# Kernel optimization log

Measured on AMD Instinct MI355X. Metric: run time of the kernel, lower is better.

Reference implementation:

```python
import jax, jax.numpy as jnp
import numpy as np

E = 8        # n_experts
TOP_K = 2    # top_k_experts


def setup_inputs() -> dict:
    key = jax.random.key(0)
    ks = jax.random.split(key, 4)
    B, N, D, H = 4, 2048, 1024, 1024
    s_d = 1.0 / np.sqrt(D)
    s_h = 1.0 / np.sqrt(H)
    return {
        "x": jax.random.normal(ks[0], (B, N, D), dtype=jnp.float32),
        "router_w": jax.random.normal(ks[1], (E, D), dtype=jnp.float32) * s_d,
        "router_b": jnp.zeros((E,), dtype=jnp.float32),
        "W_up": jax.random.normal(ks[2], (E, D, H), dtype=jnp.float32) * s_d,
        "b_up": jnp.zeros((E, H), dtype=jnp.float32),
        "W_down": jax.random.normal(ks[3], (E, H, D), dtype=jnp.float32) * s_h,
        "b_down": jnp.zeros((E, D), dtype=jnp.float32),
    }


def reference(x, router_w, router_b, W_up, b_up, W_down, b_down):
    # Router logits: (B, N, E)
    logits = jnp.einsum("bnd,ed->bne", x, router_w) + router_b
    _, topk_idx = jax.lax.top_k(logits, TOP_K)          # (B, N, K)
    # Boolean mask of selected experts: (B, N, E)
    mask = jax.nn.one_hot(topk_idx, E, dtype=jnp.bool_).any(axis=-2)
    masked_logits = jnp.where(mask, logits, -jnp.inf)
    router_weights = jax.nn.softmax(masked_logits, axis=-1)  # zeros off top-k
    # Dense all-experts FFN: (B, N, E, H) intermediate
    h = jnp.einsum("bnd,edh->bneh", x, W_up) + b_up
    h = jax.nn.gelu(h, approximate=False)  # torch F.gelu default = exact erf
    h = jnp.einsum("bneh,ehd->bned", h, W_down) + b_down
    output = jnp.einsum("bne,bned->bnd", router_weights, h)
    # Switch load-balancing aux loss (dropout is identity in eval)
    f_i = mask.astype(x.dtype).mean(axis=(0, 1))
    P_i = router_weights.mean(axis=(0, 1))
    aux_loss = E * jnp.sum(f_i * P_i)
    return output, aux_loss
```

## Files before the change

kernel.cpp:

```cpp
#include <hip/hip_runtime.h>
#include <hip/hip_bf16.h>

typedef __attribute__((ext_vector_type(8))) short bf16x8_t;
typedef __attribute__((ext_vector_type(4))) float f32x4_t;

__device__ __forceinline__ void gld16(void* lds, const void* g) {
    __builtin_amdgcn_global_load_lds(
        (const __attribute__((address_space(1))) void*)g,
        (__attribute__((address_space(3))) void*)lds, 16, 0, 0);
}

__device__ inline unsigned short f2bf(float f) {
    __hip_bfloat16 h = __float2bfloat16(f);
    return *reinterpret_cast<unsigned short*>(&h);
}

__global__ __launch_bounds__(256) void transpose_kernel(
    const float* __restrict__ Wup, const float* __restrict__ Wdn,
    ushort* __restrict__ WtUp, ushort* __restrict__ WtDn)
{
    int z = blockIdx.z;
    const float* src = (z < 8) ? (Wup + ((size_t)z << 20)) : (Wdn + ((size_t)(z - 8) << 20));
    ushort* dst      = (z < 8) ? (WtUp + ((size_t)z << 20)) : (WtDn + ((size_t)(z - 8) << 20));
    __shared__ float tile[64][65];
    int x0 = blockIdx.x * 64, y0 = blockIdx.y * 64;
    int row = threadIdx.x >> 4, colq = threadIdx.x & 15;
#pragma unroll
    for (int it = 0; it < 4; it++) {
        int r = row + it * 16;
        float4 v = *(const float4*)(src + (size_t)(y0 + r) * 1024 + x0 + colq * 4);
        tile[r][colq * 4 + 0] = v.x; tile[r][colq * 4 + 1] = v.y;
        tile[r][colq * 4 + 2] = v.z; tile[r][colq * 4 + 3] = v.w;
    }
    __syncthreads();
#pragma unroll
    for (int it = 0; it < 4; it++) {
        int r = row + it * 16;
        ushort4 o;
        o.x = f2bf(tile[colq * 4 + 0][r]); o.y = f2bf(tile[colq * 4 + 1][r]);
        o.z = f2bf(tile[colq * 4 + 2][r]); o.w = f2bf(tile[colq * 4 + 3][r]);
        *(ushort4*)(dst + (size_t)(x0 + r) * 1024 + y0 + colq * 4) = o;
    }
}

__global__ __launch_bounds__(256) void router_kernel(
    const float* __restrict__ x, const float* __restrict__ rw,
    const float* __restrict__ rb, ushort* __restrict__ xb,
    int2* __restrict__ tok_e, float2* __restrict__ tok_w)
{
    int wave = threadIdx.x >> 6, lane = threadIdx.x & 63;
    int t = blockIdx.x * 4 + wave;
    float4 xv[4];
#pragma unroll
    for (int i = 0; i < 4; i++)
        xv[i] = *(const float4*)(x + (size_t)t * 1024 + i * 256 + lane * 4);
#pragma unroll
    for (int i = 0; i < 4; i++) {
        ushort4 o;
        o.x = f2bf(xv[i].x); o.y = f2bf(xv[i].y); o.z = f2bf(xv[i].z); o.w = f2bf(xv[i].w);
        *(ushort4*)(xb + (size_t)t * 1024 + i * 256 + lane * 4) = o;
    }
    float logit[8];
#pragma unroll
    for (int e = 0; e < 8; e++) {
        float s = 0.f;
#pragma unroll
        for (int i = 0; i < 4; i++) {
            float4 wv = *(const float4*)(rw + e * 1024 + i * 256 + lane * 4);
            s += xv[i].x * wv.x + xv[i].y * wv.y + xv[i].z * wv.z + xv[i].w * wv.w;
        }
#pragma unroll
        for (int m = 32; m >= 1; m >>= 1) s += __shfl_xor(s, m, 64);
        logit[e] = s + rb[e];
    }
    int i0 = 0;
#pragma unroll
    for (int e = 1; e < 8; e++) if (logit[e] > logit[i0]) i0 = e;
    int i1 = -1;
#pragma unroll
    for (int e = 0; e < 8; e++) if (e != i0 && (i1 < 0 || logit[e] > logit[i1])) i1 = e;
    float ev = expf(logit[i1] - logit[i0]);
    float s = 1.f + ev;
    if (lane == 0) {
        tok_e[t] = make_int2(i0, i1);
        tok_w[t] = make_float2(1.f / s, ev / s);
    }
}

__global__ __launch_bounds__(256) void count_kernel(
    const int2* __restrict__ tok_e, const float2* __restrict__ tok_w,
    int* __restrict__ blockCnt, float* __restrict__ blockSum)
{
    __shared__ int lcnt[8];
    __shared__ float lsum[8];
    int tid = threadIdx.x;
    if (tid < 8) { lcnt[tid] = 0; lsum[tid] = 0.f; }
    __syncthreads();
    int t = blockIdx.x * 256 + tid;
    int2 e = tok_e[t]; float2 w = tok_w[t];
    atomicAdd(&lcnt[e.x], 1); atomicAdd(&lsum[e.x], w.x);
    atomicAdd(&lcnt[e.y], 1); atomicAdd(&lsum[e.y], w.y);
    __syncthreads();
    if (tid < 8) {
        blockCnt[blockIdx.x * 8 + tid] = lcnt[tid];
        blockSum[blockIdx.x * 8 + tid] = lsum[tid];
    }
}

__global__ void scan_kernel(const int* __restrict__ blockCnt,
                            const float* __restrict__ blockSum,
                            int* __restrict__ cnt, int* __restrict__ off,
                            int* __restrict__ base, int* __restrict__ tileE,
                            int* __restrict__ tileRow, int* __restrict__ nTiles,
                            float* aux_out)
{
    if (threadIdx.x == 0) {
        int tot[8]; float sw[8];
        for (int e = 0; e < 8; e++) { tot[e] = 0; sw[e] = 0.f; }
        for (int b = 0; b < 32; b++)
            for (int e = 0; e < 8; e++) { tot[e] += blockCnt[b * 8 + e]; sw[e] += blockSum[b * 8 + e]; }
        int o = 0; float aux = 0.f; int nT = 0;
        for (int e = 0; e < 8; e++) {
            cnt[e] = tot[e]; off[e] = o;
            aux += (float)tot[e] * sw[e];
            int run = o;
            for (int b = 0; b < 32; b++) { base[b * 8 + e] = run; run += blockCnt[b * 8 + e]; }
            for (int tt = 0; tt * 128 < tot[e]; tt++) { tileE[nT] = e; tileRow[nT] = o + tt * 128; nT++; }
            o += tot[e];
        }
        *nTiles = nT;
        aux *= 8.0f / (8192.0f * 8192.0f);
        *aux_out = aux;
    }
}

__global__ __launch_bounds__(256) void assign_kernel(
    const int2* __restrict__ tok_e, const float2* __restrict__ tok_w,
    const int* __restrict__ base, int* __restrict__ pair_token,
    float* __restrict__ pair_w, int2* __restrict__ tokSlot)
{
    __shared__ int lcnt[8];
    int tid = threadIdx.x;
    if (tid < 8) lcnt[tid] = 0;
    __syncthreads();
    int t = blockIdx.x * 256 + tid;
    int2 e = tok_e[t]; float2 w = tok_w[t];
    int r0 = atomicAdd(&lcnt[e.x], 1);
    int r1 = atomicAdd(&lcnt[e.y], 1);
    int s0 = base[blockIdx.x * 8 + e.x] + r0;
    int s1 = base[blockIdx.x * 8 + e.y] + r1;
    pair_token[s0] = t; pair_w[s0] = w.x;
    pair_token[s1] = t; pair_w[s1] = w.y;
    tokSlot[t] = make_int2(s0, s1);
}

__global__ __launch_bounds__(512, 4) void up_gemm(
    const ushort* __restrict__ xb, const ushort* __restrict__ WtUp,
    const float* __restrict__ bup,
    const int* __restrict__ cnt, const int* __restrict__ off,
    const int* __restrict__ nTiles, const int* __restrict__ tileE,
    const int* __restrict__ tileRow,
    const int* __restrict__ pair_token, const float* __restrict__ pair_w,
    const ushort* __restrict__ zeroPage, ushort* __restrict__ Hbuf)
{
    if ((int)blockIdx.y >= *nTiles) return;
    int e = tileE[blockIdx.y];
    int rowBase = tileRow[blockIdx.y];
    int expertEnd = off[e] + cnt[e];
    int colBase = blockIdx.x * 128;
    const ushort* Bsrc = WtUp + ((size_t)e << 20);

    __shared__ ushort As[128 * 32];
    __shared__ ushort Bs[128 * 32];

    int tid = threadIdx.x, w = tid >> 6, lane = tid & 63;
    int q = lane >> 4, r = lane & 15;
    int wm = w & 3, wn = w >> 2;

    int sr = lane >> 2;
    int cOff = (lane & 3) * 8;
    int rA = w * 16 + sr;
    int gA = rowBase + rA;

    const ushort* aP = (gA < expertEnd) ? xb + (size_t)pair_token[gA] * 1024 + cOff : zeroPage + cOff;
    const ushort* bP = Bsrc + (size_t)(colBase + rA) * 1024 + cOff;

    ushort* lA = &As[(w * 16) * 32];
    ushort* lB = &Bs[(w * 16) * 32];

    f32x4_t acc[2][4];
#pragma unroll
    for (int i = 0; i < 2; i++)
#pragma unroll
        for (int j = 0; j < 4; j++) { acc[i][j][0] = 0.f; acc[i][j][1] = 0.f; acc[i][j][2] = 0.f; acc[i][j][3] = 0.f; }

    for (int kk = 0; kk < 1024; kk += 32) {
        gld16(lA, aP + kk);
        gld16(lB, bP + kk);
        __syncthreads();
        bf16x8_t a[2], b[4];
#pragma unroll
        for (int i = 0; i < 2; i++) a[i] = *(const bf16x8_t*)&As[(wm * 32 + i * 16 + r) * 32 + q * 8];
#pragma unroll
        for (int j = 0; j < 4; j++) b[j] = *(const bf16x8_t*)&Bs[(wn * 64 + j * 16 + r) * 32 + q * 8];
#pragma unroll
        for (int i = 0; i < 2; i++)
#pragma unroll
            for (int j = 0; j < 4; j++)
                acc[i][j] = __builtin_amdgcn_mfma_f32_16x16x32_bf16(a[i], b[j], acc[i][j], 0, 0, 0);
        __syncthreads();
    }

#pragma unroll
    for (int j = 0; j < 4; j++) {
        int col = colBase + wn * 64 + j * 16 + r;
        float bias = bup[e * 1024 + col];
#pragma unroll
        for (int i = 0; i < 2; i++) {
#pragma unroll
            for (int reg = 0; reg < 4; reg++) {
                int gRow = rowBase + wm * 32 + i * 16 + q * 4 + reg;
                if (gRow < expertEnd) {
                    float h = acc[i][j][reg] + bias;
                    float g = 0.5f * h * (1.0f + erff(h * 0.70710678118654752f));
                    Hbuf[(size_t)gRow * 1024 + col] = f2bf(g * pair_w[gRow]);
                }
            }
        }
    }
}

__global__ __launch_bounds__(512, 4) void down_gemm(
    const ushort* __restrict__ Hbuf, const ushort* __restrict__ WtDn,
    const int* __restrict__ cnt, const int* __restrict__ off,
    const int* __restrict__ nTiles, const int* __restrict__ tileE,
    const int* __restrict__ tileRow,
    const ushort* __restrict__ zeroPage, ushort* __restrict__ pairOut)
{
    if ((int)blockIdx.y >= *nTiles) return;
    int e = tileE[blockIdx.y];
    int rowBase = tileRow[blockIdx.y];
    int expertEnd = off[e] + cnt[e];
    int colBase = blockIdx.x * 128;
    const ushort* Bsrc = WtDn + ((size_t)e << 20);

    __shared__ ushort As[128 * 32];
    __shared__ ushort Bs[128 * 32];

    int tid = threadIdx.x, w = tid >> 6, lane = tid & 63;
    int q = lane >> 4, r = lane & 15;
    int wm = w & 3, wn = w >> 2;

    int sr = lane >> 2;
    int cOff = (lane & 3) * 8;
    int rA = w * 16 + sr;
    int gA = rowBase + rA;

    const ushort* aP = (gA < expertEnd) ? Hbuf + (size_t)gA * 1024 + cOff : zeroPage + cOff;
    const ushort* bP = Bsrc + (size_t)(colBase + rA) * 1024 + cOff;

    ushort* lA = &As[(w * 16) * 32];
    ushort* lB = &Bs[(w * 16) * 32];

    f32x4_t acc[2][4];
#pragma unroll
    for (int i = 0; i < 2; i++)
#pragma unroll
        for (int j = 0; j < 4; j++) { acc[i][j][0] = 0.f; acc[i][j][1] = 0.f; acc[i][j][2] = 0.f; acc[i][j][3] = 0.f; }

    for (int kk = 0; kk < 1024; kk += 32) {
        gld16(lA, aP + kk);
        gld16(lB, bP + kk);
        __syncthreads();
        bf16x8_t a[2], b[4];
#pragma unroll
        for (int i = 0; i < 2; i++) a[i] = *(const bf16x8_t*)&As[(wm * 32 + i * 16 + r) * 32 + q * 8];
#pragma unroll
        for (int j = 0; j < 4; j++) b[j] = *(const bf16x8_t*)&Bs[(wn * 64 + j * 16 + r) * 32 + q * 8];
#pragma unroll
        for (int i = 0; i < 2; i++)
#pragma unroll
            for (int j = 0; j < 4; j++)
                acc[i][j] = __builtin_amdgcn_mfma_f32_16x16x32_bf16(a[i], b[j], acc[i][j], 0, 0, 0);
        __syncthreads();
    }

#pragma unroll
    for (int j = 0; j < 4; j++) {
        int col = colBase + wn * 64 + j * 16 + r;
#pragma unroll
        for (int i = 0; i < 2; i++) {
#pragma unroll
            for (int reg = 0; reg < 4; reg++) {
                int gRow = rowBase + wm * 32 + i * 16 + q * 4 + reg;
                if (gRow < expertEnd)
                    pairOut[(size_t)gRow * 1024 + col] = f2bf(acc[i][j][reg]);
            }
        }
    }
}

__global__ __launch_bounds__(256) void finalize_kernel(
    const ushort* __restrict__ pairOut, const int2* __restrict__ tokSlot,
    const int2* __restrict__ tok_e, const float2* __restrict__ tok_w,
    const float* __restrict__ bdn, float* __restrict__ out)
{
    int t = blockIdx.x;
    int2 s = tokSlot[t]; int2 e = tok_e[t]; float2 w = tok_w[t];
    int c = threadIdx.x * 4;
    ushort4 p0 = *(const ushort4*)(pairOut + (size_t)s.x * 1024 + c);
    ushort4 p1 = *(const ushort4*)(pairOut + (size_t)s.y * 1024 + c);
    float4 b0 = *(const float4*)(bdn + (size_t)e.x * 1024 + c);
    float4 b1 = *(const float4*)(bdn + (size_t)e.y * 1024 + c);
    __hip_bfloat16* h0 = (__hip_bfloat16*)&p0;
    __hip_bfloat16* h1 = (__hip_bfloat16*)&p1;
    float4 o;
    o.x = __bfloat162float(h0[0]) + __bfloat162float(h1[0]) + w.x * b0.x + w.y * b1.x;
    o.y = __bfloat162float(h0[1]) + __bfloat162float(h1[1]) + w.x * b0.y + w.y * b1.y;
    o.z = __bfloat162float(h0[2]) + __bfloat162float(h1[2]) + w.x * b0.z + w.y * b1.z;
    o.w = __bfloat162float(h0[3]) + __bfloat162float(h1[3]) + w.x * b0.w + w.y * b1.w;
    *(float4*)(out + (size_t)t * 1024 + c) = o;
}

extern "C" void kernel_launch(void* const* d_in, const int* in_sizes, int n_in,
                              void* d_out, int out_size, void* d_ws, size_t ws_size,
                              hipStream_t stream) {
    const float* x   = (const float*)d_in[0];
    const float* rw  = (const float*)d_in[1];
    const float* rb  = (const float*)d_in[2];
    const float* Wup = (const float*)d_in[3];
    const float* bup = (const float*)d_in[4];
    const float* Wdn = (const float*)d_in[5];
    const float* bdn = (const float*)d_in[6];
    float* out = (float*)d_out;

    char* ws = (char*)d_ws;
    int*    cnt      = (int*)(ws + 0);
    int*    off      = (int*)(ws + 64);
    int*    nTiles   = (int*)(ws + 128);
    int*    blockCnt = (int*)(ws + 256);
    float*  blockSum = (float*)(ws + 1536);
    int*    base     = (int*)(ws + 2816);
    int*    tileE    = (int*)(ws + 4096);
    int*    tileRow  = (int*)(ws + 4736);
    ushort* zeroPage = (ushort*)(ws + 8192);
    int2*   tok_e    = (int2*)(ws + 12288);
    float2* tok_w    = (float2*)(ws + 77824);
    int2*   tokSlot  = (int2*)(ws + 143360);
    int*    pair_token = (int*)(ws + 208896);
    float*  pair_w     = (float*)(ws + 274432);
    char* big = ws + 1048576;
    ushort* Hbuf    = (ushort*)big;
    ushort* pairOut = (ushort*)(big + 33554432);
    ushort* WtUp    = (ushort*)(big + 67108864);
    ushort* WtDn    = (ushort*)(big + 83886080);
    ushort* xb      = (ushort*)(big + 100663296);

    hipMemsetAsync(zeroPage, 0, 4096, stream);

    transpose_kernel<<<dim3(16, 16, 16), 256, 0, stream>>>(Wup, Wdn, WtUp, WtDn);
    router_kernel<<<2048, 256, 0, stream>>>(x, rw, rb, xb, tok_e, tok_w);
    count_kernel<<<32, 256, 0, stream>>>(tok_e, tok_w, blockCnt, blockSum);
    scan_kernel<<<1, 64, 0, stream>>>(blockCnt, blockSum, cnt, off, base,
                                      tileE, tileRow, nTiles, out + 8388608);
    assign_kernel<<<32, 256, 0, stream>>>(tok_e, tok_w, base, pair_token, pair_w, tokSlot);
    up_gemm<<<dim3(8, 136), 512, 0, stream>>>(
        xb, WtUp, bup, cnt, off, nTiles, tileE, tileRow, pair_token, pair_w, zeroPage, Hbuf);
    down_gemm<<<dim3(8, 136), 512, 0, stream>>>(
        Hbuf, WtDn, cnt, off, nTiles, tileE, tileRow, zeroPage, pairOut);
    finalize_kernel<<<8192, 256, 0, stream>>>(pairOut, tokSlot, tok_e, tok_w, bdn, out);
}
```

Measured before the change: 345.6 us.

## Double-buffer LDS in expert GEMMs, enlarge per-warp tiles, stage epilogue through LDS

```diff
diff --git a/kernel.cpp b/kernel.cpp
--- a/kernel.cpp
+++ b/kernel.cpp
@@ -154,7 +154,14 @@
     tokSlot[t] = make_int2(s0, s1);
 }
 
-__global__ __launch_bounds__(512, 4) void up_gemm(
+#define STAGE(buf, kk_) do {                               \
+    gld16(&As[buf][(w * 16) * 32],        aP0 + (kk_));    \
+    gld16(&As[buf][(64 + w * 16) * 32],   aP1 + (kk_));    \
+    gld16(&Bs[buf][(w * 16) * 32],        bP0 + (kk_));    \
+    gld16(&Bs[buf][(64 + w * 16) * 32],   bP1 + (kk_));    \
+} while (0)
+
+__global__ __launch_bounds__(256) void up_gemm(
     const ushort* __restrict__ xb, const ushort* __restrict__ WtUp,
     const float* __restrict__ bup,
     const int* __restrict__ cnt, const int* __restrict__ off,
@@ -170,67 +177,81 @@
     int colBase = blockIdx.x * 128;
     const ushort* Bsrc = WtUp + ((size_t)e << 20);
 
-    __shared__ ushort As[128 * 32];
-    __shared__ ushort Bs[128 * 32];
+    __shared__ __align__(16) ushort smem[17408];
+    ushort (*As)[4096] = (ushort (*)[4096])smem;
+    ushort (*Bs)[4096] = (ushort (*)[4096])(smem + 8192);
 
     int tid = threadIdx.x, w = tid >> 6, lane = tid & 63;
     int q = lane >> 4, r = lane & 15;
-    int wm = w & 3, wn = w >> 2;
+    int wm = w & 1, wn = w >> 1;
 
     int sr = lane >> 2;
     int cOff = (lane & 3) * 8;
-    int rA = w * 16 + sr;
-    int gA = rowBase + rA;
-
-    const ushort* aP = (gA < expertEnd) ? xb + (size_t)pair_token[gA] * 1024 + cOff : zeroPage + cOff;
-    const ushort* bP = Bsrc + (size_t)(colBase + rA) * 1024 + cOff;
-
-    ushort* lA = &As[(w * 16) * 32];
-    ushort* lB = &Bs[(w * 16) * 32];
-
-    f32x4_t acc[2][4];
-#pragma unroll
-    for (int i = 0; i < 2; i++)
+    int rA0 = w * 16 + sr, rA1 = 64 + w * 16 + sr;
+    int gA0 = rowBase + rA0, gA1 = rowBase + rA1;
+
+    const ushort* aP0 = (gA0 < expertEnd) ? xb + (size_t)pair_token[gA0] * 1024 + cOff : zeroPage + cOff;
+    const ushort* aP1 = (gA1 < expertEnd) ? xb + (size_t)pair_token[gA1] * 1024 + cOff : zeroPage + cOff;
+    const ushort* bP0 = Bsrc + (size_t)(colBase + rA0) * 1024 + cOff;
+    const ushort* bP1 = Bsrc + (size_t)(colBase + rA1) * 1024 + cOff;
+
+    f32x4_t acc[4][4];
+#pragma unroll
+    for (int i = 0; i < 4; i++)
 #pragma unroll
         for (int j = 0; j < 4; j++) { acc[i][j][0] = 0.f; acc[i][j][1] = 0.f; acc[i][j][2] = 0.f; acc[i][j][3] = 0.f; }
 
+    STAGE(0, 0);
+    __syncthreads();
+    int cur = 0;
+#pragma unroll 2
     for (int kk = 0; kk < 1024; kk += 32) {
-        gld16(lA, aP + kk);
-        gld16(lB, bP + kk);
-        __syncthreads();
-        bf16x8_t a[2], b[4];
-#pragma unroll
-        for (int i = 0; i < 2; i++) a[i] = *(const bf16x8_t*)&As[(wm * 32 + i * 16 + r) * 32 + q * 8];
-#pragma unroll
-        for (int j = 0; j < 4; j++) b[j] = *(const bf16x8_t*)&Bs[(wn * 64 + j * 16 + r) * 32 + q * 8];
-#pragma unroll
-        for (int i = 0; i < 2; i++)
+        if (kk + 32 < 1024) STAGE(cur ^ 1, kk + 32);
+        bf16x8_t a[4], b[4];
+#pragma unroll
+        for (int i = 0; i < 4; i++) a[i] = *(const bf16x8_t*)&As[cur][(wm * 64 + i * 16 + r) * 32 + q * 8];
+#pragma unroll
+        for (int j = 0; j < 4; j++) b[j] = *(const bf16x8_t*)&Bs[cur][(wn * 64 + j * 16 + r) * 32 + q * 8];
+#pragma unroll
+        for (int i = 0; i < 4; i++)
 #pragma unroll
             for (int j = 0; j < 4; j++)
                 acc[i][j] = __builtin_amdgcn_mfma_f32_16x16x32_bf16(a[i], b[j], acc[i][j], 0, 0, 0);
         __syncthreads();
-    }
-
-#pragma unroll
-    for (int j = 0; j < 4; j++) {
-        int col = colBase + wn * 64 + j * 16 + r;
-        float bias = bup[e * 1024 + col];
-#pragma unroll
-        for (int i = 0; i < 2; i++) {
-#pragma unroll
-            for (int reg = 0; reg < 4; reg++) {
-                int gRow = rowBase + wm * 32 + i * 16 + q * 4 + reg;
-                if (gRow < expertEnd) {
-                    float h = acc[i][j][reg] + bias;
-                    float g = 0.5f * h * (1.0f + erff(h * 0.70710678118654752f));
-                    Hbuf[(size_t)gRow * 1024 + col] = f2bf(g * pair_w[gRow]);
-                }
+        cur ^= 1;
+    }
+
+    float biasv[4];
+#pragma unroll
+    for (int j = 0; j < 4; j++) biasv[j] = bup[e * 1024 + colBase + wn * 64 + j * 16 + r];
+#pragma unroll
+    for (int i = 0; i < 4; i++) {
+#pragma unroll
+        for (int reg = 0; reg < 4; reg++) {
+            int rt = wm * 64 + i * 16 + q * 4 + reg;
+            int gRow = rowBase + rt;
+            float pw = (gRow < expertEnd) ? pair_w[gRow] : 0.f;
+#pragma unroll
+            for (int j = 0; j < 4; j++) {
+                float h = acc[i][j][reg] + biasv[j];
+                float g = 0.5f * h * (1.0f + erff(h * 0.70710678118654752f));
+                smem[rt * 136 + wn * 64 + j * 16 + r] = f2bf(g * pw);
             }
         }
     }
-}
-
-__global__ __launch_bounds__(512, 4) void down_gemm(
+    __syncthreads();
+#pragma unroll
+    for (int n = 0; n < 8; n++) {
+        int rt = n * 16 + (tid >> 4);
+        int gRow = rowBase + rt;
+        if (gRow < expertEnd) {
+            bf16x8_t v = *(const bf16x8_t*)&smem[rt * 136 + (tid & 15) * 8];
+            *(bf16x8_t*)(Hbuf + (size_t)gRow * 1024 + colBase + (tid & 15) * 8) = v;
+        }
+    }
+}
+
+__global__ __launch_bounds__(256) void down_gemm(
     const ushort* __restrict__ Hbuf, const ushort* __restrict__ WtDn,
     const int* __restrict__ cnt, const int* __restrict__ off,
     const int* __restrict__ nTiles, const int* __restrict__ tileE,
@@ -244,58 +265,68 @@
     int colBase = blockIdx.x * 128;
     const ushort* Bsrc = WtDn + ((size_t)e << 20);
 
-    __shared__ ushort As[128 * 32];
-    __shared__ ushort Bs[128 * 32];
+    __shared__ __align__(16) ushort smem[17408];
+    ushort (*As)[4096] = (ushort (*)[4096])smem;
+    ushort (*Bs)[4096] = (ushort (*)[4096])(smem + 8192);
 
     int tid = threadIdx.x, w = tid >> 6, lane = tid & 63;
     int q = lane >> 4, r = lane & 15;
-    int wm = w & 3, wn = w >> 2;
+    int wm = w & 1, wn = w >> 1;
 
     int sr = lane >> 2;
     int cOff = (lane & 3) * 8;
-    int rA = w * 16 + sr;
-    int gA = rowBase + rA;
-
-    const ushort* aP = (gA < expertEnd) ? Hbuf + (size_t)gA * 1024 + cOff : zeroPage + cOff;
-    const ushort* bP = Bsrc + (size_t)(colBase + rA) * 1024 + cOff;
-
-    ushort* lA = &As[(w * 16) * 32];
-    ushort* lB = &Bs[(w * 16) * 32];
-
-    f32x4_t acc[2][4];
-#pragma unroll
-    for (int i = 0; i < 2; i++)
+    int rA0 = w * 16 + sr, rA1 = 64 + w * 16 + sr;
+    int gA0 = rowBase + rA0, gA1 = rowBase + rA1;
+
+    const ushort* aP0 = (gA0 < expertEnd) ? Hbuf + (size_t)gA0 * 1024 + cOff : zeroPage + cOff;
+    const ushort* aP1 = (gA1 < expertEnd) ? Hbuf + (size_t)gA1 * 1024 + cOff : zeroPage + cOff;
+    const ushort* bP0 = Bsrc + (size_t)(colBase + rA0) * 1024 + cOff;
+    const ushort* bP1 = Bsrc + (size_t)(colBase + rA1) * 1024 + cOff;
+
+    f32x4_t acc[4][4];
+#pragma unroll
+    for (int i = 0; i < 4; i++)
 #pragma unroll
         for (int j = 0; j < 4; j++) { acc[i][j][0] = 0.f; acc[i][j][1] = 0.f; acc[i][j][2] = 0.f; acc[i][j][3] = 0.f; }
 
+    STAGE(0, 0);
+    __syncthreads();
+    int cur = 0;
+#pragma unroll 2
     for (int kk = 0; kk < 1024; kk += 32) {
-        gld16(lA, aP + kk);
-        gld16(lB, bP + kk);
-        __syncthreads();
-        bf16x8_t a[2], b[4];
-#pragma unroll
-        for (int i = 0; i < 2; i++) a[i] = *(const bf16x8_t*)&As[(wm * 32 + i * 16 + r) * 32 + q * 8];
-#pragma unroll
-        for (int j = 0; j < 4; j++) b[j] = *(const bf16x8_t*)&Bs[(wn * 64 + j * 16 + r) * 32 + q * 8];
-#pragma unroll
-        for (int i = 0; i < 2; i++)
+        if (kk + 32 < 1024) STAGE(cur ^ 1, kk + 32);
+        bf16x8_t a[4], b[4];
+#pragma unroll
+        for (int i = 0; i < 4; i++) a[i] = *(const bf16x8_t*)&As[cur][(wm * 64 + i * 16 + r) * 32 + q * 8];
+#pragma unroll
+        for (int j = 0; j < 4; j++) b[j] = *(const bf16x8_t*)&Bs[cur][(wn * 64 + j * 16 + r) * 32 + q * 8];
+#pragma unroll
+        for (int i = 0; i < 4; i++)
 #pragma unroll
             for (int j = 0; j < 4; j++)
                 acc[i][j] = __builtin_amdgcn_mfma_f32_16x16x32_bf16(a[i], b[j], acc[i][j], 0, 0, 0);
         __syncthreads();
-    }
-
-#pragma unroll
-    for (int j = 0; j < 4; j++) {
-        int col = colBase + wn * 64 + j * 16 + r;
-#pragma unroll
-        for (int i = 0; i < 2; i++) {
-#pragma unroll
-            for (int reg = 0; reg < 4; reg++) {
-                int gRow = rowBase + wm * 32 + i * 16 + q * 4 + reg;
-                if (gRow < expertEnd)
-                    pairOut[(size_t)gRow * 1024 + col] = f2bf(acc[i][j][reg]);
-            }
+        cur ^= 1;
+    }
+
+#pragma unroll
+    for (int i = 0; i < 4; i++) {
+#pragma unroll
+        for (int reg = 0; reg < 4; reg++) {
+            int rt = wm * 64 + i * 16 + q * 4 + reg;
+#pragma unroll
+            for (int j = 0; j < 4; j++)
+                smem[rt * 136 + wn * 64 + j * 16 + r] = f2bf(acc[i][j][reg]);
+        }
+    }
+    __syncthreads();
+#pragma unroll
+    for (int n = 0; n < 8; n++) {
+        int rt = n * 16 + (tid >> 4);
+        int gRow = rowBase + rt;
+        if (gRow < expertEnd) {
+            bf16x8_t v = *(const bf16x8_t*)&smem[rt * 136 + (tid & 15) * 8];
+            *(bf16x8_t*)(pairOut + (size_t)gRow * 1024 + colBase + (tid & 15) * 8) = v;
         }
     }
 }
@@ -364,9 +395,9 @@
     scan_kernel<<<1, 64, 0, stream>>>(blockCnt, blockSum, cnt, off, base,
                                       tileE, tileRow, nTiles, out + 8388608);
     assign_kernel<<<32, 256, 0, stream>>>(tok_e, tok_w, base, pair_token, pair_w, tokSlot);
-    up_gemm<<<dim3(8, 136), 512, 0, stream>>>(
+    up_gemm<<<dim3(8, 136), 256, 0, stream>>>(
         xb, WtUp, bup, cnt, off, nTiles, tileE, tileRow, pair_token, pair_w, zeroPage, Hbuf);
-    down_gemm<<<dim3(8, 136), 512, 0, stream>>>(
+    down_gemm<<<dim3(8, 136), 256, 0, stream>>>(
         Hbuf, WtDn, cnt, off, nTiles, tileE, tileRow, zeroPage, pairOut);
     finalize_kernel<<<8192, 256, 0, stream>>>(pairOut, tokSlot, tok_e, tok_w, bdn, out);
 }
```

Result: faster. 331.1 us (-4.2%).
